# Performance work log

Hardware: AMD Instinct MI355X
Metric: run time of the kernel (lower is better)

## Reference

```python
import jax, jax.numpy as jnp
import numpy as np

N, P, D, FDIM, TFEAT = 65536, 6, 256, 8, 16
RAW_DIM = 4 + TFEAT  # 20
IN_DIM = 3 + FDIM + 3 + 3  # xyz + frame embedding + rigid xyz + viewdir = 17


def setup_inputs() -> dict:
    key = jax.random.key(0)
    ks = jax.random.split(key, 16)
    inp = {
        "tpts": jax.random.normal(ks[0], (N, P, 3), jnp.float32),
        "bigpts": jax.random.normal(ks[1], (N, P, 3), jnp.float32),
        "viewdir": jax.random.normal(ks[2], (N, P, 3), jnp.float32),
        "dists": jax.random.uniform(ks[3], (N,), jnp.float32),
        "part_dist": jax.random.uniform(ks[4], (1, N, P), jnp.float32),
        "frame_dim": jax.random.normal(ks[5], (FDIM,), jnp.float32),
        "W1": jax.random.normal(ks[6], (P, IN_DIM, D), jnp.float32) / np.sqrt(IN_DIM),
        "b1": jax.random.normal(ks[7], (P, D), jnp.float32) * 0.01,
        "W2": jax.random.normal(ks[8], (P, D, D), jnp.float32) / np.sqrt(D),
        "b2": jax.random.normal(ks[9], (P, D), jnp.float32) * 0.01,
        "W3": jax.random.normal(ks[10], (P, D, RAW_DIM), jnp.float32) / np.sqrt(D),
        "b3": jax.random.normal(ks[11], (P, RAW_DIM), jnp.float32) * 0.01,
        "Wocc": jax.random.normal(ks[12], (P, D, 1), jnp.float32) / np.sqrt(D),
        "bocc": jax.random.normal(ks[13], (P, 1), jnp.float32) * 0.01,
        "tflag": jax.random.randint(ks[14], (N, P), 0, 2).astype(bool),
    }
    return inp


def _part_mlps(tpts, bigpts, viewdir, frame_dim, W1, b1, W2, b2, W3, b3, Wocc, bocc):
    # Run all P part networks on all N points (batched per-part GEMMs).
    n = tpts.shape[0]
    frame = jnp.broadcast_to(frame_dim, (n, P, FDIM))
    x = jnp.concatenate([tpts, frame, bigpts, viewdir], axis=-1)  # (N,P,17)
    h = jax.nn.relu(jnp.einsum('npi,pid->npd', x, W1) + b1)
    h = jax.nn.relu(jnp.einsum('npd,pde->npe', h, W2) + b2)
    raw_p = jnp.einsum('npd,pdr->npr', h, W3) + b3               # (N,P,20)
    occ_p = jax.nn.sigmoid(jnp.einsum('npd,pdo->npo', h, Wocc) + bocc)  # (N,P,1)
    return raw_p, occ_p


def reference(tpts, bigpts, viewdir, dists, part_dist, frame_dim,
              W1, b1, W2, b2, W3, b3, Wocc, bocc, tflag):
    raw_p, occ_p = _part_mlps(tpts, bigpts, viewdir, frame_dim,
                              W1, b1, W2, b2, W3, b3, Wocc, bocc)
    # scatter-back equivalent: unflagged (point, part) slots stay zero
    flag = tflag[..., None].astype(raw_p.dtype)  # (N,P,1)
    raws = raw_p * flag                           # (N,P,20)
    occs = occ_p * flag                           # (N,P,1)
    # cfg.aggr == 'mean'
    raw = raws.mean(axis=1)                       # (N,20)
    occ = occs.mean(axis=1)                       # (N,1)
    tocc = occs[..., 0]                           # (N,P)
    return jnp.concatenate([raw, occ, tocc], axis=-1)  # (N, 20+1+P)
```

## Files before the change

### kernel.cpp

```cpp
#include <hip/hip_runtime.h>
#include <hip/hip_bf16.h>

using bf16 = __hip_bfloat16;
typedef __bf16 bf16x8 __attribute__((ext_vector_type(8)));
typedef __bf16 bf16x4v __attribute__((ext_vector_type(4)));
typedef float f32x4 __attribute__((ext_vector_type(4)));

#define MFMA16(a, b, c) __builtin_amdgcn_mfma_f32_16x16x32_bf16((a), (b), (c), 0, 0, 0)

__device__ __forceinline__ void bar_lds() {
  asm volatile("s_waitcnt lgkmcnt(0)" ::: "memory");
  __builtin_amdgcn_s_barrier();
}


__global__ void prep_kernel(const float* __restrict__ W1, const float* __restrict__ b1,
                            const float* __restrict__ W2, const float* __restrict__ W3,
                            const float* __restrict__ Wocc, __bf16* __restrict__ ws) {
  const int b = blockIdx.x;
  const int tid = threadIdx.x;
  if (b < 96) {
    __shared__ float tile[64][65];
    const int p = b >> 4, t = b & 15;
    const int d0 = (t >> 2) * 64, e0 = (t & 3) * 64;
    const int lane = tid & 63, grp = tid >> 6;
    const float* src = W2 + p * 65536 + (d0 + grp * 16) * 256 + e0 + lane;
#pragma unroll
    for (int i = 0; i < 16; ++i) tile[grp * 16 + i][lane] = src[i * 256];
    __syncthreads();
#pragma unroll
    for (int q = 0; q < 2; ++q) {
      const int m = tid + q * 256;
      const int ee = m >> 3, c = m & 7;
      bf16x8 v;
#pragma unroll
      for (int j = 0; j < 8; ++j) v[j] = (__bf16)tile[c * 8 + j][ee];
      *reinterpret_cast<bf16x8*>(
          &ws[49152 + p * 65536 + (e0 + ee) * 256 + d0 + c * 8]) = v;
    }
    return;
  }
  const int t = 49152 + (b - 96) * 256 + tid;
  if (t < 55296) {
    const int u = t - 49152;
    const int p = u >> 10, r = u & 1023, n = r >> 2, c = r & 3;
    bf16x8 v;
#pragma unroll
    for (int j = 0; j < 8; ++j) {
      const int k = c * 8 + j;
      float x = 0.f;
      if (k < 17) {
        const int ko = (k < 8) ? k + 3 : ((k < 11) ? k - 8 : k);
        x = W1[p * 4352 + ko * 256 + n];
      } else if (k == 17) {
        x = b1[p * 256 + n];
      }
      v[j] = (__bf16)x;
    }
    *reinterpret_cast<bf16x8*>(&ws[p * 8192 + n * 32 + c * 8]) = v;
  } else if (t < 61440) {
    const int u = t - 55296;
    const int p = u >> 10, r = u & 1023, row = r >> 5, c = r & 31;
    bf16x8 v;
#pragma unroll
    for (int j = 0; j < 8; ++j) {
      const int k = c * 8 + j;
      float x = 0.f;
      if (row < 20)       x = W3[p * 5120 + k * 20 + row];
      else if (row == 20) x = Wocc[p * 256 + k];
      v[j] = (__bf16)x;
    }
    *reinterpret_cast<bf16x8*>(&ws[442368 + p * 8192 + row * 256 + c * 8]) = v;
  }
}

__global__ __launch_bounds__(512, 4) void tpose_main(
    const float* __restrict__ tpts, const float* __restrict__ bigpts,
    const float* __restrict__ viewdir, const float* __restrict__ frame,
    const float* __restrict__ b2g, const float* __restrict__ b3g,
    const float* __restrict__ boccg, const int* __restrict__ tflag,
    const __bf16* __restrict__ ws, float* __restrict__ out) {
  const __bf16* __restrict__ W1t = ws;
  const __bf16* __restrict__ W2t = ws + 49152;
  const __bf16* __restrict__ W3t = ws + 442368;

  __shared__ __align__(16) __bf16 Xf[128 * 40];
  __shared__ __align__(16) __bf16 Hf[128 * 256];
  __shared__ float Tocc[128 * 6];

  const int tid = threadIdx.x;
  const int w = tid >> 6;
  const int lane = tid & 63;
  const int lq = lane >> 4;
  const int ln = lane & 15;
  const int e = ln & 7;
  const int n0 = blockIdx.x * 128;

  if (tid < 128) {
    bf16x8 f8;
#pragma unroll
    for (int j = 0; j < 8; ++j) f8[j] = (__bf16)frame[j];
    *reinterpret_cast<bf16x8*>(&Xf[tid * 40]) = f8;
    bf16x8 z = {};
    z[1] = (__bf16)1.0f;
    *reinterpret_cast<bf16x8*>(&Xf[tid * 40 + 16]) = z;
    bf16x8 z2 = {};
    *reinterpret_cast<bf16x8*>(&Xf[tid * 40 + 24]) = z2;
  }

  const int role = tid & 3;
  const int ppt = tid >> 2;
  const float* __restrict__ dynsrc =
      (role == 0) ? tpts : (role == 1) ? bigpts : viewdir;

  float pre[3];
  {
    const int base3 = (n0 + ppt) * 18;
#pragma unroll
    for (int i = 0; i < 3; ++i) pre[i] = dynsrc[base3 + i];
  }
  float flv = (tflag[(n0 + w * 16 + ln) * 6] != 0) ? 1.f : 0.f;

  float psum0[4] = {0.f, 0.f, 0.f, 0.f};
  float psum1[4] = {0.f, 0.f, 0.f, 0.f};

  for (int p = 0; p < 6; ++p) {
    if (role < 3) {
#pragma unroll
      for (int i = 0; i < 3; ++i)
        Xf[ppt * 40 + 8 + role * 3 + i] = (__bf16)pre[i];
    }

    bf16x8 aw[2];
#pragma unroll
    for (int mt = 0; mt < 2; ++mt)
      aw[mt] = *reinterpret_cast<const bf16x8*>(
          &W1t[p * 8192 + (w * 32 + mt * 16 + ln) * 32 + lq * 8]);

    bar_lds();

    f32x4 acc[2][8];
#pragma unroll
    for (int mt = 0; mt < 2; ++mt)
#pragma unroll
      for (int nt = 0; nt < 8; ++nt) acc[mt][nt] = f32x4{0.f, 0.f, 0.f, 0.f};
#pragma unroll
    for (int nt = 0; nt < 8; ++nt) {
      const bf16x8 xb =
          *reinterpret_cast<const bf16x8*>(&Xf[(nt * 16 + ln) * 40 + lq * 8]);
#pragma unroll
      for (int mt = 0; mt < 2; ++mt) acc[mt][nt] = MFMA16(aw[mt], xb, acc[mt][nt]);
    }
#pragma unroll
    for (int mt = 0; mt < 2; ++mt) {
      const int c = w * 4 + mt * 2 + (lq >> 1);
      const int off = ((c ^ e) << 3) + (lq & 1) * 4;
#pragma unroll
      for (int nt = 0; nt < 8; ++nt) {
        bf16x4v hv;
#pragma unroll
        for (int r = 0; r < 4; ++r) hv[r] = (__bf16)fmaxf(acc[mt][nt][r], 0.f);
        *reinterpret_cast<bf16x4v*>(&Hf[(nt * 16 + ln) * 256 + off]) = hv;
      }
    }

    bar_lds();

    const __bf16* __restrict__ w2p = W2t + p * 65536 + (w * 32 + ln) * 256 + lq * 8;
    bf16x8 a2[2];
#pragma unroll
    for (int mt = 0; mt < 2; ++mt)
      a2[mt] = *reinterpret_cast<const bf16x8*>(w2p + mt * 4096);
    f32x4 b2v[2];
#pragma unroll
    for (int mt = 0; mt < 2; ++mt)
      b2v[mt] = *reinterpret_cast<const f32x4*>(
          &b2g[p * 256 + w * 32 + mt * 16 + lq * 4]);

    const int pn = (p < 5) ? p + 1 : 5;
    {
      const int base3 = ((n0 + ppt) * 6 + pn) * 3;
#pragma unroll
      for (int i = 0; i < 3; ++i) pre[i] = dynsrc[base3 + i];
    }
    const float fln = (tflag[(n0 + w * 16 + ln) * 6 + pn] != 0) ? 1.f : 0.f;

#pragma unroll
    for (int mt = 0; mt < 2; ++mt)
#pragma unroll
      for (int nt = 0; nt < 8; ++nt) acc[mt][nt] = b2v[mt];

#pragma unroll 1
    for (int kk = 0; kk < 8; ++kk) {
      bf16x8 a2n[2];
      if (kk < 7) {
#pragma unroll
        for (int mt = 0; mt < 2; ++mt)
          a2n[mt] = *reinterpret_cast<const bf16x8*>(
              w2p + mt * 4096 + (kk + 1) * 32);
      }
      const int off = ((kk * 4 + lq) ^ e) << 3;
      {
        bf16x8 hb[4];
#pragma unroll
        for (int nt = 0; nt < 4; ++nt)
          hb[nt] = *reinterpret_cast<const bf16x8*>(
              &Hf[(nt * 16 + ln) * 256 + off]);
#pragma unroll
        for (int nt = 0; nt < 4; ++nt)
#pragma unroll
          for (int mt = 0; mt < 2; ++mt)
            acc[mt][nt] = MFMA16(a2[mt], hb[nt], acc[mt][nt]);
      }
      __builtin_amdgcn_sched_barrier(0);
      {
        bf16x8 hb[4];
#pragma unroll
        for (int nt = 0; nt < 4; ++nt)
          hb[nt] = *reinterpret_cast<const bf16x8*>(
              &Hf[((nt + 4) * 16 + ln) * 256 + off]);
#pragma unroll
        for (int nt = 0; nt < 4; ++nt)
#pragma unroll
          for (int mt = 0; mt < 2; ++mt)
            acc[mt][nt + 4] = MFMA16(a2[mt], hb[nt], acc[mt][nt + 4]);
      }
#pragma unroll
      for (int mt = 0; mt < 2; ++mt) a2[mt] = a2n[mt];
    }

    bar_lds();

#pragma unroll
    for (int mt = 0; mt < 2; ++mt) {
      const int c = w * 4 + mt * 2 + (lq >> 1);
      const int off = ((c ^ e) << 3) + (lq & 1) * 4;
#pragma unroll
      for (int nt = 0; nt < 8; ++nt) {
        bf16x4v hv;
#pragma unroll
        for (int r = 0; r < 4; ++r) hv[r] = (__bf16)fmaxf(acc[mt][nt][r], 0.f);
        *reinterpret_cast<bf16x4v*>(&Hf[(nt * 16 + ln) * 256 + off]) = hv;
      }
    }

    bar_lds();

    f32x4 acc3[2];
    {
#pragma unroll
      for (int mt = 0; mt < 2; ++mt)
#pragma unroll
        for (int r = 0; r < 4; ++r) {
          const int d = mt * 16 + lq * 4 + r;
          float v = 0.f;
          if (d < 20)       v = b3g[p * 20 + d];
          else if (d == 20) v = boccg[p];
          acc3[mt][r] = v;
        }
    }
    const __bf16* __restrict__ w3p = W3t + p * 8192 + ln * 256 + lq * 8;
#pragma unroll 2
    for (int kk = 0; kk < 8; ++kk) {
      bf16x8 a3[2];
#pragma unroll
      for (int mt = 0; mt < 2; ++mt)
        a3[mt] = *reinterpret_cast<const bf16x8*>(w3p + mt * 4096 + kk * 32);
      const bf16x8 hb = *reinterpret_cast<const bf16x8*>(
          &Hf[(w * 16 + ln) * 256 + (((kk * 4 + lq) ^ e) << 3)]);
#pragma unroll
      for (int mt = 0; mt < 2; ++mt) acc3[mt] = MFMA16(a3[mt], hb, acc3[mt]);
    }

#pragma unroll
    for (int r = 0; r < 4; ++r) psum0[r] += flv * acc3[0][r];
    if (lq == 0) {
#pragma unroll
      for (int r = 0; r < 4; ++r) psum1[r] += flv * acc3[1][r];
    } else if (lq == 1) {
      const float occ = 1.f / (1.f + __expf(-acc3[1][0]));
      Tocc[(w * 16 + ln) * 6 + p] = flv * occ;
      psum1[0] += flv * occ;
    }

    flv = fln;
  }

  bar_lds();
  float* stage = reinterpret_cast<float*>(Hf);
  const float inv6 = 1.f / 6.f;
  {
    const int ptl = w * 16 + ln;
#pragma unroll
    for (int r = 0; r < 4; ++r) stage[ptl * 27 + lq * 4 + r] = psum0[r] * inv6;
    if (lq == 0) {
#pragma unroll
      for (int r = 0; r < 4; ++r) stage[ptl * 27 + 16 + r] = psum1[r] * inv6;
    } else if (lq == 1) {
      stage[ptl * 27 + 20] = psum1[0] * inv6;
    }
  }
  if (tid < 128) {
#pragma unroll
    for (int pp = 0; pp < 6; ++pp) stage[tid * 27 + 21 + pp] = Tocc[tid * 6 + pp];
  }
  bar_lds();
  float* outp = out + (size_t)n0 * 27;
#pragma unroll
  for (int q = 0; q < 2; ++q) {
    const int m = tid + q * 512;
    if (m < 864)
      *reinterpret_cast<f32x4*>(&outp[m * 4]) =
          *reinterpret_cast<const f32x4*>(&stage[m * 4]);
  }
}

extern "C" void kernel_launch(void* const* d_in, const int* in_sizes, int n_in,
                              void* d_out, int out_size, void* d_ws, size_t ws_size,
                              hipStream_t stream) {
  const float* tpts    = (const float*)d_in[0];
  const float* bigpts  = (const float*)d_in[1];
  const float* viewdir = (const float*)d_in[2];
  const float* frame   = (const float*)d_in[5];
  const float* W1      = (const float*)d_in[6];
  const float* b1      = (const float*)d_in[7];
  const float* W2      = (const float*)d_in[8];
  const float* b2      = (const float*)d_in[9];
  const float* W3      = (const float*)d_in[10];
  const float* b3      = (const float*)d_in[11];
  const float* Wocc    = (const float*)d_in[12];
  const float* bocc    = (const float*)d_in[13];
  const int*   tflag   = (const int*)d_in[14];
  __bf16* ws  = (__bf16*)d_ws;
  float*  out = (float*)d_out;

  prep_kernel<<<144, 256, 0, stream>>>(W1, b1, W2, W3, Wocc, ws);
  tpose_main<<<512, 512, 0, stream>>>(tpts, bigpts, viewdir, frame, b2, b3,
                                      bocc, tflag, ws, out);
}
```

Before: 197.3 us.

## Switch to 32x32x16 MFMA tiles with 4-wave blocks per 128 points

Replaces the 16x16x32 bf16 MFMA tiling with 32x32x16 MFMA tiles in all three layers. Blocks shrink from 8 to 4 waves, so each wave now owns 64 hidden rows and 32 points. The larger instruction is meant to cut the number of MFMA issues and the LDS B-operand reads per FLOP. It also adds s_setprio around the W2 loop. The cost is more accumulator registers per wave (128 floats) and fewer waves to hide latency, which may lower occupancy.

```diff
diff --git a/kernel.cpp b/kernel.cpp
--- a/kernel.cpp
+++ b/kernel.cpp
@@ -5,8 +5,9 @@
 typedef __bf16 bf16x8 __attribute__((ext_vector_type(8)));
 typedef __bf16 bf16x4v __attribute__((ext_vector_type(4)));
 typedef float f32x4 __attribute__((ext_vector_type(4)));
-
-#define MFMA16(a, b, c) __builtin_amdgcn_mfma_f32_16x16x32_bf16((a), (b), (c), 0, 0, 0)
+typedef float f32x16 __attribute__((ext_vector_type(16)));
+
+#define MFMA32(a, b, c) __builtin_amdgcn_mfma_f32_32x32x16_bf16((a), (b), (c), 0, 0, 0)
 
 __device__ __forceinline__ void bar_lds() {
   asm volatile("s_waitcnt lgkmcnt(0)" ::: "memory");
@@ -74,7 +75,7 @@
   }
 }
 
-__global__ __launch_bounds__(512, 4) void tpose_main(
+__global__ __launch_bounds__(256, 2) void tpose_main(
     const float* __restrict__ tpts, const float* __restrict__ bigpts,
     const float* __restrict__ viewdir, const float* __restrict__ frame,
     const float* __restrict__ b2g, const float* __restrict__ b3g,
@@ -91,10 +92,11 @@
   const int tid = threadIdx.x;
   const int w = tid >> 6;
   const int lane = tid & 63;
-  const int lq = lane >> 4;
-  const int ln = lane & 15;
-  const int e = ln & 7;
+  const int ln5 = lane & 31;
+  const int hi = lane >> 5;
+  const int e5 = ln5 & 7;
   const int n0 = blockIdx.x * 128;
+  const int ptD = w * 32 + ln5;
 
   if (tid < 128) {
     bf16x8 f8;
@@ -109,178 +111,187 @@
   }
 
   const int role = tid & 3;
-  const int ppt = tid >> 2;
   const float* __restrict__ dynsrc =
       (role == 0) ? tpts : (role == 1) ? bigpts : viewdir;
 
-  float pre[3];
-  {
-    const int base3 = (n0 + ppt) * 18;
-#pragma unroll
-    for (int i = 0; i < 3; ++i) pre[i] = dynsrc[base3 + i];
-  }
-  float flv = (tflag[(n0 + w * 16 + ln) * 6] != 0) ? 1.f : 0.f;
-
-  float psum0[4] = {0.f, 0.f, 0.f, 0.f};
-  float psum1[4] = {0.f, 0.f, 0.f, 0.f};
+  float pre[2][3];
+#pragma unroll
+  for (int pass = 0; pass < 2; ++pass) {
+    const int pt = (tid >> 2) + pass * 64;
+    const int base3 = (n0 + pt) * 18;
+#pragma unroll
+    for (int i = 0; i < 3; ++i) pre[pass][i] = dynsrc[base3 + i];
+  }
+  float flv = (tflag[(n0 + ptD) * 6] != 0) ? 1.f : 0.f;
+
+  float psum[12];
+#pragma unroll
+  for (int k = 0; k < 12; ++k) psum[k] = 0.f;
 
   for (int p = 0; p < 6; ++p) {
     if (role < 3) {
 #pragma unroll
-      for (int i = 0; i < 3; ++i)
-        Xf[ppt * 40 + 8 + role * 3 + i] = (__bf16)pre[i];
-    }
-
-    bf16x8 aw[2];
-#pragma unroll
-    for (int mt = 0; mt < 2; ++mt)
-      aw[mt] = *reinterpret_cast<const bf16x8*>(
-          &W1t[p * 8192 + (w * 32 + mt * 16 + ln) * 32 + lq * 8]);
+      for (int pass = 0; pass < 2; ++pass) {
+        const int pt = (tid >> 2) + pass * 64;
+#pragma unroll
+        for (int i = 0; i < 3; ++i)
+          Xf[pt * 40 + 8 + role * 3 + i] = (__bf16)pre[pass][i];
+      }
+    }
+
+    bf16x8 aw[2][2];
+#pragma unroll
+    for (int mt = 0; mt < 2; ++mt)
+#pragma unroll
+      for (int kt = 0; kt < 2; ++kt)
+        aw[mt][kt] = *reinterpret_cast<const bf16x8*>(
+            &W1t[p * 8192 + (w * 64 + mt * 32 + ln5) * 32 + kt * 16 + hi * 8]);
 
     bar_lds();
 
-    f32x4 acc[2][8];
-#pragma unroll
-    for (int mt = 0; mt < 2; ++mt)
-#pragma unroll
-      for (int nt = 0; nt < 8; ++nt) acc[mt][nt] = f32x4{0.f, 0.f, 0.f, 0.f};
-#pragma unroll
-    for (int nt = 0; nt < 8; ++nt) {
-      const bf16x8 xb =
-          *reinterpret_cast<const bf16x8*>(&Xf[(nt * 16 + ln) * 40 + lq * 8]);
-#pragma unroll
-      for (int mt = 0; mt < 2; ++mt) acc[mt][nt] = MFMA16(aw[mt], xb, acc[mt][nt]);
-    }
-#pragma unroll
-    for (int mt = 0; mt < 2; ++mt) {
-      const int c = w * 4 + mt * 2 + (lq >> 1);
-      const int off = ((c ^ e) << 3) + (lq & 1) * 4;
-#pragma unroll
-      for (int nt = 0; nt < 8; ++nt) {
-        bf16x4v hv;
-#pragma unroll
-        for (int r = 0; r < 4; ++r) hv[r] = (__bf16)fmaxf(acc[mt][nt][r], 0.f);
-        *reinterpret_cast<bf16x4v*>(&Hf[(nt * 16 + ln) * 256 + off]) = hv;
-      }
-    }
+    f32x16 acc[2][4];
+#pragma unroll
+    for (int mt = 0; mt < 2; ++mt)
+#pragma unroll
+      for (int nt = 0; nt < 4; ++nt)
+#pragma unroll
+        for (int k = 0; k < 16; ++k) acc[mt][nt][k] = 0.f;
+#pragma unroll
+    for (int nt = 0; nt < 4; ++nt)
+#pragma unroll
+      for (int kt = 0; kt < 2; ++kt) {
+        const bf16x8 xb = *reinterpret_cast<const bf16x8*>(
+            &Xf[(nt * 32 + ln5) * 40 + kt * 16 + hi * 8]);
+#pragma unroll
+        for (int mt = 0; mt < 2; ++mt)
+          acc[mt][nt] = MFMA32(aw[mt][kt], xb, acc[mt][nt]);
+      }
+#pragma unroll
+    for (int mt = 0; mt < 2; ++mt)
+#pragma unroll
+      for (int q = 0; q < 4; ++q) {
+        const int off = (((w * 8 + mt * 4 + q) ^ e5) << 3) + hi * 4;
+#pragma unroll
+        for (int nt = 0; nt < 4; ++nt) {
+          bf16x4v hv;
+#pragma unroll
+          for (int r = 0; r < 4; ++r)
+            hv[r] = (__bf16)fmaxf(acc[mt][nt][q * 4 + r], 0.f);
+          *reinterpret_cast<bf16x4v*>(&Hf[(nt * 32 + ln5) * 256 + off]) = hv;
+        }
+      }
 
     bar_lds();
 
-    const __bf16* __restrict__ w2p = W2t + p * 65536 + (w * 32 + ln) * 256 + lq * 8;
+    const __bf16* __restrict__ w2p =
+        W2t + p * 65536 + (w * 64 + ln5) * 256 + hi * 8;
     bf16x8 a2[2];
 #pragma unroll
     for (int mt = 0; mt < 2; ++mt)
-      a2[mt] = *reinterpret_cast<const bf16x8*>(w2p + mt * 4096);
-    f32x4 b2v[2];
-#pragma unroll
-    for (int mt = 0; mt < 2; ++mt)
-      b2v[mt] = *reinterpret_cast<const f32x4*>(
-          &b2g[p * 256 + w * 32 + mt * 16 + lq * 4]);
+      a2[mt] = *reinterpret_cast<const bf16x8*>(w2p + mt * 8192);
+    f32x4 b2q[2][4];
+#pragma unroll
+    for (int mt = 0; mt < 2; ++mt)
+#pragma unroll
+      for (int q = 0; q < 4; ++q)
+        b2q[mt][q] = *reinterpret_cast<const f32x4*>(
+            &b2g[p * 256 + w * 64 + mt * 32 + q * 8 + hi * 4]);
 
     const int pn = (p < 5) ? p + 1 : 5;
-    {
-      const int base3 = ((n0 + ppt) * 6 + pn) * 3;
-#pragma unroll
-      for (int i = 0; i < 3; ++i) pre[i] = dynsrc[base3 + i];
-    }
-    const float fln = (tflag[(n0 + w * 16 + ln) * 6 + pn] != 0) ? 1.f : 0.f;
-
-#pragma unroll
-    for (int mt = 0; mt < 2; ++mt)
-#pragma unroll
-      for (int nt = 0; nt < 8; ++nt) acc[mt][nt] = b2v[mt];
-
+#pragma unroll
+    for (int pass = 0; pass < 2; ++pass) {
+      const int pt = (tid >> 2) + pass * 64;
+      const int base3 = ((n0 + pt) * 6 + pn) * 3;
+#pragma unroll
+      for (int i = 0; i < 3; ++i) pre[pass][i] = dynsrc[base3 + i];
+    }
+    const float fln = (tflag[(n0 + ptD) * 6 + pn] != 0) ? 1.f : 0.f;
+
+#pragma unroll
+    for (int mt = 0; mt < 2; ++mt)
+#pragma unroll
+      for (int nt = 0; nt < 4; ++nt)
+#pragma unroll
+        for (int q = 0; q < 4; ++q)
+#pragma unroll
+          for (int r = 0; r < 4; ++r)
+            acc[mt][nt][q * 4 + r] = b2q[mt][q][r];
+
+    __builtin_amdgcn_s_setprio(1);
 #pragma unroll 1
-    for (int kk = 0; kk < 8; ++kk) {
+    for (int kt = 0; kt < 16; ++kt) {
       bf16x8 a2n[2];
-      if (kk < 7) {
+      if (kt < 15) {
 #pragma unroll
         for (int mt = 0; mt < 2; ++mt)
           a2n[mt] = *reinterpret_cast<const bf16x8*>(
-              w2p + mt * 4096 + (kk + 1) * 32);
-      }
-      const int off = ((kk * 4 + lq) ^ e) << 3;
-      {
-        bf16x8 hb[4];
-#pragma unroll
-        for (int nt = 0; nt < 4; ++nt)
-          hb[nt] = *reinterpret_cast<const bf16x8*>(
-              &Hf[(nt * 16 + ln) * 256 + off]);
-#pragma unroll
-        for (int nt = 0; nt < 4; ++nt)
-#pragma unroll
-          for (int mt = 0; mt < 2; ++mt)
-            acc[mt][nt] = MFMA16(a2[mt], hb[nt], acc[mt][nt]);
-      }
-      __builtin_amdgcn_sched_barrier(0);
-      {
-        bf16x8 hb[4];
-#pragma unroll
-        for (int nt = 0; nt < 4; ++nt)
-          hb[nt] = *reinterpret_cast<const bf16x8*>(
-              &Hf[((nt + 4) * 16 + ln) * 256 + off]);
-#pragma unroll
-        for (int nt = 0; nt < 4; ++nt)
-#pragma unroll
-          for (int mt = 0; mt < 2; ++mt)
-            acc[mt][nt + 4] = MFMA16(a2[mt], hb[nt], acc[mt][nt + 4]);
-      }
+              w2p + mt * 8192 + (kt + 1) * 16);
+      }
+      const int off = ((kt * 2 + hi) ^ e5) << 3;
+      bf16x8 hb[4];
+#pragma unroll
+      for (int nt = 0; nt < 4; ++nt)
+        hb[nt] = *reinterpret_cast<const bf16x8*>(
+            &Hf[(nt * 32 + ln5) * 256 + off]);
+#pragma unroll
+      for (int nt = 0; nt < 4; ++nt)
+#pragma unroll
+        for (int mt = 0; mt < 2; ++mt)
+          acc[mt][nt] = MFMA32(a2[mt], hb[nt], acc[mt][nt]);
 #pragma unroll
       for (int mt = 0; mt < 2; ++mt) a2[mt] = a2n[mt];
     }
+    __builtin_amdgcn_s_setprio(0);
 
     bar_lds();
 
 #pragma unroll
-    for (int mt = 0; mt < 2; ++mt) {
-      const int c = w * 4 + mt * 2 + (lq >> 1);
-      const int off = ((c ^ e) << 3) + (lq & 1) * 4;
-#pragma unroll
-      for (int nt = 0; nt < 8; ++nt) {
-        bf16x4v hv;
-#pragma unroll
-        for (int r = 0; r < 4; ++r) hv[r] = (__bf16)fmaxf(acc[mt][nt][r], 0.f);
-        *reinterpret_cast<bf16x4v*>(&Hf[(nt * 16 + ln) * 256 + off]) = hv;
-      }
-    }
+    for (int mt = 0; mt < 2; ++mt)
+#pragma unroll
+      for (int q = 0; q < 4; ++q) {
+        const int off = (((w * 8 + mt * 4 + q) ^ e5) << 3) + hi * 4;
+#pragma unroll
+        for (int nt = 0; nt < 4; ++nt) {
+          bf16x4v hv;
+#pragma unroll
+          for (int r = 0; r < 4; ++r)
+            hv[r] = (__bf16)fmaxf(acc[mt][nt][q * 4 + r], 0.f);
+          *reinterpret_cast<bf16x4v*>(&Hf[(nt * 32 + ln5) * 256 + off]) = hv;
+        }
+      }
 
     bar_lds();
 
-    f32x4 acc3[2];
-    {
-#pragma unroll
-      for (int mt = 0; mt < 2; ++mt)
-#pragma unroll
-        for (int r = 0; r < 4; ++r) {
-          const int d = mt * 16 + lq * 4 + r;
-          float v = 0.f;
-          if (d < 20)       v = b3g[p * 20 + d];
-          else if (d == 20) v = boccg[p];
-          acc3[mt][r] = v;
-        }
-    }
-    const __bf16* __restrict__ w3p = W3t + p * 8192 + ln * 256 + lq * 8;
-#pragma unroll 2
-    for (int kk = 0; kk < 8; ++kk) {
-      bf16x8 a3[2];
-#pragma unroll
-      for (int mt = 0; mt < 2; ++mt)
-        a3[mt] = *reinterpret_cast<const bf16x8*>(w3p + mt * 4096 + kk * 32);
+    f32x16 acc3;
+#pragma unroll
+    for (int q = 0; q < 4; ++q)
+#pragma unroll
+      for (int r = 0; r < 4; ++r) {
+        const int d = q * 8 + hi * 4 + r;
+        float v = 0.f;
+        if (d < 20)       v = b3g[p * 20 + d];
+        else if (d == 20) v = boccg[p];
+        acc3[q * 4 + r] = v;
+      }
+    const __bf16* __restrict__ w3p = W3t + p * 8192 + ln5 * 256 + hi * 8;
+#pragma unroll 4
+    for (int kt = 0; kt < 16; ++kt) {
+      const bf16x8 a3 = *reinterpret_cast<const bf16x8*>(w3p + kt * 16);
       const bf16x8 hb = *reinterpret_cast<const bf16x8*>(
-          &Hf[(w * 16 + ln) * 256 + (((kk * 4 + lq) ^ e) << 3)]);
-#pragma unroll
-      for (int mt = 0; mt < 2; ++mt) acc3[mt] = MFMA16(a3[mt], hb, acc3[mt]);
-    }
-
-#pragma unroll
-    for (int r = 0; r < 4; ++r) psum0[r] += flv * acc3[0][r];
-    if (lq == 0) {
-#pragma unroll
-      for (int r = 0; r < 4; ++r) psum1[r] += flv * acc3[1][r];
-    } else if (lq == 1) {
-      const float occ = 1.f / (1.f + __expf(-acc3[1][0]));
-      Tocc[(w * 16 + ln) * 6 + p] = flv * occ;
-      psum1[0] += flv * occ;
+          &Hf[ptD * 256 + (((kt * 2 + hi) ^ e5) << 3)]);
+      acc3 = MFMA32(a3, hb, acc3);
+    }
+
+#pragma unroll
+    for (int k = 0; k < 12; ++k) {
+      const int d = (k >> 2) * 8 + hi * 4 + (k & 3);
+      if (d < 20) {
+        psum[k] += flv * acc3[k];
+      } else if (d == 20) {
+        const float occ = 1.f / (1.f + __expf(-acc3[k]));
+        Tocc[ptD * 6 + p] = flv * occ;
+        psum[k] += flv * occ;
+      }
     }
 
     flv = fln;
@@ -289,16 +300,10 @@
   bar_lds();
   float* stage = reinterpret_cast<float*>(Hf);
   const float inv6 = 1.f / 6.f;
-  {
-    const int ptl = w * 16 + ln;
-#pragma unroll
-    for (int r = 0; r < 4; ++r) stage[ptl * 27 + lq * 4 + r] = psum0[r] * inv6;
-    if (lq == 0) {
-#pragma unroll
-      for (int r = 0; r < 4; ++r) stage[ptl * 27 + 16 + r] = psum1[r] * inv6;
-    } else if (lq == 1) {
-      stage[ptl * 27 + 20] = psum1[0] * inv6;
-    }
+#pragma unroll
+  for (int k = 0; k < 12; ++k) {
+    const int d = (k >> 2) * 8 + hi * 4 + (k & 3);
+    if (d <= 20) stage[ptD * 27 + d] = psum[k] * inv6;
   }
   if (tid < 128) {
 #pragma unroll
@@ -307,8 +312,8 @@
   bar_lds();
   float* outp = out + (size_t)n0 * 27;
 #pragma unroll
-  for (int q = 0; q < 2; ++q) {
-    const int m = tid + q * 512;
+  for (int q = 0; q < 4; ++q) {
+    const int m = tid + q * 256;
     if (m < 864)
       *reinterpret_cast<f32x4*>(&outp[m * 4]) =
           *reinterpret_cast<const f32x4*>(&stage[m * 4]);
@@ -335,6 +340,6 @@
   float*  out = (float*)d_out;
 
   prep_kernel<<<144, 256, 0, stream>>>(W1, b1, W2, W3, Wocc, ws);
-  tpose_main<<<512, 512, 0, stream>>>(tpts, bigpts, viewdir, frame, b2, b3,
+  tpose_main<<<512, 256, 0, stream>>>(tpts, bigpts, viewdir, frame, b2, b3,
                                       bocc, tflag, ws, out);
 }
```

Measured after the change: 183.8 us. -6.8%, faster.
